# Kernel tuning notes

Measured on AMD Instinct MI355X. Metric: run time of the kernel, lower is better.

Reference implementation:

```python
import jax, jax.numpy as jnp
import numpy as np

B, C, H, W = 4, 512, 56, 56
G, K = 16, 3
P = K * K
GC = C // G
DWK = 3
PAD = 1
OFFSET_SCALE = 1.0


def setup_inputs():
    key = jax.random.key(0)
    ks = jax.random.split(key, 10)

    def w(i, shape, sc=0.02):
        return jax.random.normal(ks[i], shape, jnp.float32) * sc

    return {
        "x": jax.random.normal(ks[0], (B, C, H, W), jnp.float32),
        "w_in": w(1, (C, C)), "b_in": jnp.zeros((C,), jnp.float32),
        "w_dw": w(2, (DWK, DWK, 1, C)), "b_dw": jnp.zeros((C,), jnp.float32),
        "ln_g": jnp.ones((C,), jnp.float32), "ln_b": jnp.zeros((C,), jnp.float32),
        "w_off": w(3, (C, G * P * 2)), "b_off": jnp.zeros((G * P * 2,), jnp.float32),
        "w_mask": w(4, (C, G * P)), "b_mask": jnp.zeros((G * P,), jnp.float32),
        "w_out": w(5, (C, C)), "b_out": jnp.zeros((C,), jnp.float32),
        "bn_g": jnp.ones((C,), jnp.float32), "bn_b": jnp.zeros((C,), jnp.float32),
        "bn_m": w(6, (C,), 0.1), "bn_v": jnp.abs(w(7, (C,), 0.1)) + 1.0,
    }


def _dcnv3_core(xp, offset, mask):
    """xp: [B,H,W,C]; offset: [B,H,W,G*P*2]; mask (softmaxed over P): [B,H,W,G,P]."""
    xpad = jnp.pad(xp, ((0, 0), (PAD, PAD), (PAD, PAD), (0, 0)))
    Hin, Win = H + 2 * PAD, W + 2 * PAD
    # normalized reference points (output-location centers in padded input coords)
    ref_x = (jnp.arange(W, dtype=jnp.float32) + 0.5 + (K - 1) // 2) / Win
    ref_y = (jnp.arange(H, dtype=jnp.float32) + 0.5 + (K - 1) // 2) / Hin
    # dilation grid, kx-major / ky-minor flattening (matches InternImage core)
    k = jnp.arange(K, dtype=jnp.float32) - (K - 1) // 2
    gx = jnp.repeat(k, K) / Win  # [P]
    gy = jnp.tile(k, K) / Hin    # [P]
    off = offset.reshape(B, H, W, G, P, 2)
    lx = ref_x[None, None, :, None, None] + gx * OFFSET_SCALE + off[..., 0] * OFFSET_SCALE / Win
    ly = ref_y[None, :, None, None, None] + gy * OFFSET_SCALE + off[..., 1] * OFFSET_SCALE / Hin
    # grid_sample semantics, align_corners=False, zero padding
    px = lx * Win - 0.5
    py = ly * Hin - 0.5
    x0f = jnp.floor(px)
    y0f = jnp.floor(py)
    tx = px - x0f
    ty = py - y0f
    x0 = x0f.astype(jnp.int32)
    y0 = y0f.astype(jnp.int32)
    flat = xpad.reshape(B, Hin * Win * G, GC)
    gidx = jnp.arange(G)[None, None, :, None]

    def corner(fb, yi, xi):
        valid = (yi >= 0) & (yi < Hin) & (xi >= 0) & (xi < Win)
        idx = (jnp.clip(yi, 0, Hin - 1) * Win + jnp.clip(xi, 0, Win - 1)) * G + gidx
        return jnp.take(fb, idx, axis=0) * valid[..., None]  # [H,W,G,P,GC]

    def sample_one(fb, y0b, x0b, tyb, txb):
        w00 = ((1 - tyb) * (1 - txb))[..., None]
        w01 = ((1 - tyb) * txb)[..., None]
        w10 = (tyb * (1 - txb))[..., None]
        w11 = (tyb * txb)[..., None]
        return (corner(fb, y0b, x0b) * w00 + corner(fb, y0b, x0b + 1) * w01
                + corner(fb, y0b + 1, x0b) * w10 + corner(fb, y0b + 1, x0b + 1) * w11)

    samp = jax.vmap(sample_one)(flat, y0, x0, ty, tx)  # [B,H,W,G,P,GC]
    return jnp.einsum('bhwgpc,bhwgp->bhwgc', samp, mask).reshape(B, H, W, C)


def reference(x, w_in, b_in, w_dw, b_dw, ln_g, ln_b, w_off, b_off, w_mask, b_mask, w_out, b_out, bn_g, bn_b, bn_m, bn_v):
    xh = jnp.transpose(x, (0, 2, 3, 1))  # NCHW -> NHWC
    xp = xh @ w_in + b_in                # input_proj
    # offset/mask branch: depthwise conv + LayerNorm(channels) + GELU
    x1 = jax.lax.conv_general_dilated(xh, w_dw, (1, 1), 'SAME', feature_group_count=C,
                                      dimension_numbers=('NHWC', 'HWIO', 'NHWC')) + b_dw
    mu = x1.mean(-1, keepdims=True)
    var = x1.var(-1, keepdims=True)
    x1 = (x1 - mu) / jnp.sqrt(var + 1e-6) * ln_g + ln_b
    x1 = jax.nn.gelu(x1, approximate=False)
    offset = x1 @ w_off + b_off
    mask = jax.nn.softmax((x1 @ w_mask + b_mask).reshape(B, H, W, G, P), axis=-1)
    y = _dcnv3_core(xp, offset, mask)
    y = y @ w_out + b_out                # output_proj
    y = jnp.transpose(y, (0, 3, 1, 2))   # NHWC -> NCHW
    # BatchNorm2d (inference: running stats) + SiLU
    y = (y - bn_m[:, None, None]) / jnp.sqrt(bn_v[:, None, None] + 1e-5) * bn_g[:, None, None] + bn_b[:, None, None]
    return jax.nn.silu(y)
```

## Files before the change

kernel.cpp:

```cpp
#include <hip/hip_runtime.h>
#include <cmath>

constexpr int B_ = 4, C_ = 512, H_ = 56, W_ = 56;
constexpr int HW_ = H_ * W_;
constexpr int NPIX = B_ * HW_;
constexpr int G_ = 16, P_ = 9;
constexpr int NMSK = G_ * P_;

typedef __attribute__((ext_vector_type(8))) short short8;
typedef __attribute__((ext_vector_type(4))) float f32x4;

__device__ __forceinline__ float b2f(ushort u) {
    union { unsigned int i; float f; } v; v.i = (unsigned int)u << 16; return v.f;
}
__device__ __forceinline__ ushort f2b(float f) {
    unsigned int x = __float_as_uint(f);
    unsigned int r = (x + 0x7fffu + ((x >> 16) & 1u)) >> 16;
    return (ushort)r;
}
__device__ __forceinline__ void gload16(const ushort* g, ushort* l) {
    __builtin_amdgcn_global_load_lds(
        (const __attribute__((address_space(1))) unsigned int*)g,
        (__attribute__((address_space(3))) unsigned int*)l, 16, 0, 0);
}

__global__ __launch_bounds__(256) void prep_weights_kernel(
    const float* __restrict__ w_in, const float* __restrict__ w_off,
    const float* __restrict__ w_mask, const float* __restrict__ w_out,
    const float* __restrict__ b_off, const float* __restrict__ b_mask,
    ushort* __restrict__ wtA, ushort* __restrict__ wtOM, ushort* __restrict__ wtO,
    float* __restrict__ bOM)
{
    __shared__ float tile[32][33];
    int z = blockIdx.z;
    int k0 = blockIdx.x * 32;
    int n0 = blockIdx.y * 32;
    int tx = threadIdx.x, ty = threadIdx.y;
    for (int i = ty; i < 32; i += 8) {
        int k = k0 + i, n = n0 + tx;
        float v;
        if (z == 0) v = w_in[k * 512 + n];
        else if (z == 1) v = w_out[k * 512 + n];
        else v = (n < 288) ? w_off[k * 288 + n]
                           : (n < 432 ? w_mask[k * 144 + (n - 288)] : 0.f);
        tile[i][tx] = v;
    }
    __syncthreads();
    ushort* dst = (z == 0) ? wtA : (z == 1 ? wtO : wtOM);
    for (int i = ty; i < 32; i += 8)
        dst[(size_t)(n0 + i) * 512 + k0 + tx] = f2b(tile[tx][i]);
    if (z == 2 && blockIdx.x == 0 && blockIdx.y == 0) {
        int t = ty * 32 + tx;
        for (int tt = t; tt < 512; tt += 256)
            bOM[tt] = (tt < 288) ? b_off[tt] : (tt < 432 ? b_mask[tt - 288] : 0.f);
    }
}

__global__ __launch_bounds__(256) void transpose_in_kernel(
    const float* __restrict__ in, ushort* __restrict__ out)
{
    __shared__ float tile[32][33];
    int b = blockIdx.z;
    int hw0 = blockIdx.x * 32;
    int c0 = blockIdx.y * 32;
    int tx = threadIdx.x, ty = threadIdx.y;
    const float* ib = in + (size_t)b * C_ * HW_;
    #pragma unroll
    for (int i = ty; i < 32; i += 8)
        tile[i][tx] = ib[(size_t)(c0 + i) * HW_ + hw0 + tx];
    __syncthreads();
    ushort* ob = out + (size_t)b * HW_ * C_;
    #pragma unroll
    for (int i = ty; i < 32; i += 8)
        ob[(size_t)(hw0 + i) * C_ + c0 + tx] = f2b(tile[tx][i]);
}

template <int MODE>
__global__ __launch_bounds__(256) void mfma_gemm_kernel(
    const ushort* __restrict__ A, const ushort* __restrict__ Bt,
    const float* __restrict__ bias, void* __restrict__ Cout,
    const float* __restrict__ bng, const float* __restrict__ bnb,
    const float* __restrict__ bnm, const float* __restrict__ bnv)
{
    __shared__ ushort As[128 * 64];
    __shared__ ushort Bs[128 * 64];
    int tid = threadIdx.x;
    int lane = tid & 63, wid = tid >> 6;
    int bid = blockIdx.x;
    int wgid = (bid & 7) * 49 + (bid >> 3);
    int row0 = (wgid >> 2) * 128, col0 = (wgid & 3) * 128;
    int wm = wid >> 1, wn = wid & 1;

    f32x4 acc[4][4] = {};

    int lr = lane >> 3;
    int sc = (lane & 7) ^ lr;

    for (int k0 = 0; k0 < 512; k0 += 64) {
        if (k0) __syncthreads();
        #pragma unroll
        for (int i = 0; i < 4; i++) {
            int rb = (wid * 4 + i) * 8;
            gload16(A + (size_t)(row0 + rb + lr) * 512 + k0 + sc * 8, &As[rb * 64]);
            gload16(Bt + (size_t)(col0 + rb + lr) * 512 + k0 + sc * 8, &Bs[rb * 64]);
        }
        __syncthreads();
        #pragma unroll
        for (int ks = 0; ks < 2; ks++) {
            short8 af[4], bf[4];
            #pragma unroll
            for (int mi = 0; mi < 4; mi++) {
                int r = wm * 64 + mi * 16 + (lane & 15);
                int c = ((lane >> 4) + ks * 4) ^ (r & 7);
                af[mi] = *(const short8*)((const char*)As + r * 128 + c * 16);
            }
            #pragma unroll
            for (int ni = 0; ni < 4; ni++) {
                int r = wn * 64 + ni * 16 + (lane & 15);
                int c = ((lane >> 4) + ks * 4) ^ (r & 7);
                bf[ni] = *(const short8*)((const char*)Bs + r * 128 + c * 16);
            }
            #pragma unroll
            for (int mi = 0; mi < 4; mi++)
                #pragma unroll
                for (int ni = 0; ni < 4; ni++)
                    acc[mi][ni] = __builtin_amdgcn_mfma_f32_16x16x32_bf16(
                        af[mi], bf[ni], acc[mi][ni], 0, 0, 0);
        }
    }

    if constexpr (MODE == 2) {
        __shared__ float ebuf[4][32][67];
        int n_lane = row0 + wm * 64 + lane;
        int bb = n_lane / HW_;
        int hww = n_lane - bb * HW_;
        size_t obase = (size_t)bb * C_ * HW_ + hww;
        #pragma unroll
        for (int half = 0; half < 2; half++) {
            #pragma unroll
            for (int ni2 = 0; ni2 < 2; ni2++) {
                int ni = half * 2 + ni2;
                int col = col0 + wn * 64 + ni * 16 + (lane & 15);
                float bv = bias[col];
                float inv = rsqrtf(bnv[col] + 1e-5f);
                float bsc = bng[col] * inv;
                float bsh = bnb[col] - bnm[col] * bsc;
                int cl = ni2 * 16 + (lane & 15);
                int rl = (lane >> 4) * 4;
                #pragma unroll
                for (int mi = 0; mi < 4; mi++)
                    #pragma unroll
                    for (int r = 0; r < 4; r++) {
                        float val = acc[mi][ni][r] + bv;
                        float t2 = val * bsc + bsh;
                        float s = t2 / (1.f + expf(-t2));
                        ebuf[wid][cl][mi * 16 + rl + r] = s;
                    }
            }
            __syncthreads();
            #pragma unroll
            for (int c = 0; c < 32; c++) {
                int chan = col0 + wn * 64 + half * 32 + c;
                ((float*)Cout)[obase + (size_t)chan * HW_] = ebuf[wid][c][lane];
            }
            __syncthreads();
        }
    } else {
        #pragma unroll
        for (int ni = 0; ni < 4; ni++) {
            int col = col0 + wn * 64 + ni * 16 + (lane & 15);
            float bv = bias[col];
            #pragma unroll
            for (int mi = 0; mi < 4; mi++) {
                int rowb = row0 + wm * 64 + mi * 16 + (lane >> 4) * 4;
                #pragma unroll
                for (int r = 0; r < 4; r++) {
                    float val = acc[mi][ni][r] + bv;
                    if constexpr (MODE == 0)
                        ((float*)Cout)[(size_t)(rowb + r) * 512 + col] = val;
                    else
                        ((ushort*)Cout)[(size_t)(rowb + r) * 512 + col] = f2b(val);
                }
            }
        }
    }
}

__global__ __launch_bounds__(256) void dwln_kernel(
    const ushort* __restrict__ xh, const float* __restrict__ wdw,
    const float* __restrict__ bdw, const float* __restrict__ lng,
    const float* __restrict__ lnb, ushort* __restrict__ x1)
{
    int tid = threadIdx.x;
    int wid = tid >> 6, lane = tid & 63;
    int bid = blockIdx.x;
    int j = (bid & 7) * (NPIX / 32) + (bid >> 3);
    int n = j * 4 + wid;
    int b = n / HW_, hw = n % HW_;
    int h = hw / W_, w = hw % W_;
    int c0 = lane * 8;
    const ushort* base = xh + (size_t)b * HW_ * C_ + c0;

    uint4 nb[9];
    #pragma unroll
    for (int ky = 0; ky < 3; ky++)
        #pragma unroll
        for (int kx = 0; kx < 3; kx++) {
            int hh = h + ky - 1, ww = w + kx - 1;
            bool ok = (hh >= 0) & (hh < H_) & (ww >= 0) & (ww < W_);
            nb[ky * 3 + kx] = ok ? *(const uint4*)(base + ((size_t)hh * W_ + ww) * C_)
                                 : make_uint4(0u, 0u, 0u, 0u);
        }

    float acc[8];
    {
        float4 b0 = *(const float4*)&bdw[c0];
        float4 b1 = *(const float4*)&bdw[c0 + 4];
        acc[0] = b0.x; acc[1] = b0.y; acc[2] = b0.z; acc[3] = b0.w;
        acc[4] = b1.x; acc[5] = b1.y; acc[6] = b1.z; acc[7] = b1.w;
    }
    #pragma unroll
    for (int p = 0; p < 9; p++) {
        float4 w0 = *(const float4*)&wdw[p * C_ + c0];
        float4 w1 = *(const float4*)&wdw[p * C_ + c0 + 4];
        float wv[8] = {w0.x, w0.y, w0.z, w0.w, w1.x, w1.y, w1.z, w1.w};
        unsigned int u[4] = {nb[p].x, nb[p].y, nb[p].z, nb[p].w};
        #pragma unroll
        for (int q = 0; q < 4; q++) {
            float lo = __uint_as_float(u[q] << 16);
            float hi = __uint_as_float(u[q] & 0xffff0000u);
            acc[2 * q]     += wv[2 * q]     * lo;
            acc[2 * q + 1] += wv[2 * q + 1] * hi;
        }
    }

    float s1 = 0.f, s2 = 0.f;
    #pragma unroll
    for (int q = 0; q < 8; q++) { s1 += acc[q]; s2 += acc[q] * acc[q]; }
    #pragma unroll
    for (int o = 32; o > 0; o >>= 1) {
        s1 += __shfl_xor(s1, o);
        s2 += __shfl_xor(s2, o);
    }
    float mean = s1 * (1.f / 512.f);
    float var = s2 * (1.f / 512.f) - mean * mean;
    float inv = rsqrtf(var + 1e-6f);

    float4 g0 = *(const float4*)&lng[c0];
    float4 g1 = *(const float4*)&lng[c0 + 4];
    float4 e0 = *(const float4*)&lnb[c0];
    float4 e1 = *(const float4*)&lnb[c0 + 4];
    float gv[8] = {g0.x, g0.y, g0.z, g0.w, g1.x, g1.y, g1.z, g1.w};
    float ev[8] = {e0.x, e0.y, e0.z, e0.w, e1.x, e1.y, e1.z, e1.w};
    unsigned int outw[4];
    #pragma unroll
    for (int q = 0; q < 4; q++) {
        float t0 = (acc[2 * q]     - mean) * inv * gv[2 * q]     + ev[2 * q];
        float t1 = (acc[2 * q + 1] - mean) * inv * gv[2 * q + 1] + ev[2 * q + 1];
        float ge0 = 0.5f * t0 * (1.f + erff(t0 * 0.70710678118654752f));
        float ge1 = 0.5f * t1 * (1.f + erff(t1 * 0.70710678118654752f));
        outw[q] = (unsigned int)f2b(ge0) | ((unsigned int)f2b(ge1) << 16);
    }
    *(uint4*)&x1[(size_t)n * C_ + c0] = make_uint4(outw[0], outw[1], outw[2], outw[3]);
}

__global__ __launch_bounds__(256) void dcn_sample_kernel(
    const ushort* __restrict__ xp, const ushort* __restrict__ om,
    ushort* __restrict__ y1)
{
    __shared__ float slog[NMSK];
    __shared__ float sw4[NMSK][4];
    __shared__ int   sa4[NMSK][4];
    int bid = blockIdx.x;
    int n = (bid & 7) * (NPIX / 8) + (bid >> 3);
    int b = n / HW_, hw = n % HW_;
    int h = hw / W_, w = hw % W_;
    int tid = threadIdx.x;
    const ushort* omp = om + (size_t)n * 512;

    if (tid < NMSK) slog[tid] = b2f(omp[288 + tid]);
    __syncthreads();
    if (tid < G_) {
        float mx = -1e30f;
        #pragma unroll
        for (int p = 0; p < P_; p++) mx = fmaxf(mx, slog[tid * P_ + p]);
        float e[P_], s = 0.f;
        #pragma unroll
        for (int p = 0; p < P_; p++) { e[p] = expf(slog[tid * P_ + p] - mx); s += e[p]; }
        float invs = 1.f / s;
        #pragma unroll
        for (int p = 0; p < P_; p++) slog[tid * P_ + p] = e[p] * invs;
    }
    __syncthreads();
    if (tid < NMSK) {
        int g = tid / 9, p = tid - g * 9;
        float ox = b2f(omp[g * 18 + p * 2 + 0]);
        float oy = b2f(omp[g * 18 + p * 2 + 1]);
        float px = (float)(w + (p / 3)) + ox;
        float py = (float)(h + (p % 3)) + oy;
        float x0f = floorf(px), y0f = floorf(py);
        float tx = px - x0f, ty = py - y0f;
        int x0 = (int)x0f, y0 = (int)y0f;
        float m = slog[tid];
        float ww[4] = { (1.f - ty) * (1.f - tx) * m, (1.f - ty) * tx * m,
                        ty * (1.f - tx) * m,         ty * tx * m };
        #pragma unroll
        for (int i = 0; i < 4; i++) {
            int yy = y0 + (i >> 1), xx = x0 + (i & 1);
            bool valid = (yy >= 1 && yy <= H_ && xx >= 1 && xx <= W_);
            sa4[tid][i] = valid ? ((yy - 1) * W_ + (xx - 1)) * C_ : 0;
            sw4[tid][i] = valid ? ww[i] : 0.f;
        }
    }
    __syncthreads();

    const ushort* xpb = xp + (size_t)b * HW_ * C_;
    int c0 = tid * 2;
    int g = tid >> 4;

    int addr[P_][4];
    #pragma unroll
    for (int p = 0; p < P_; p++)
        #pragma unroll
        for (int i = 0; i < 4; i++)
            addr[p][i] = sa4[g * 9 + p][i] + c0;

    unsigned int v[P_][4];
    #pragma unroll
    for (int p = 0; p < P_; p++)
        #pragma unroll
        for (int i = 0; i < 4; i++)
            v[p][i] = *(const unsigned int*)(xpb + addr[p][i]);

    float ax = 0.f, ay = 0.f;
    #pragma unroll
    for (int p = 0; p < P_; p++)
        #pragma unroll
        for (int i = 0; i < 4; i++) {
            float wgt = sw4[g * 9 + p][i];
            float lo = __uint_as_float(v[p][i] << 16);
            float hi = __uint_as_float(v[p][i] & 0xffff0000u);
            ax += wgt * lo;
            ay += wgt * hi;
        }

    ushort2 o; o.x = f2b(ax); o.y = f2b(ay);
    *(ushort2*)&y1[(size_t)n * 512 + c0] = o;
}

extern "C" void kernel_launch(void* const* d_in, const int* in_sizes, int n_in,
                              void* d_out, int out_size, void* d_ws, size_t ws_size,
                              hipStream_t stream)
{
    const float* x      = (const float*)d_in[0];
    const float* w_in   = (const float*)d_in[1];
    const float* b_in   = (const float*)d_in[2];
    const float* w_dw   = (const float*)d_in[3];
    const float* b_dw   = (const float*)d_in[4];
    const float* ln_g   = (const float*)d_in[5];
    const float* ln_b   = (const float*)d_in[6];
    const float* w_off  = (const float*)d_in[7];
    const float* b_off  = (const float*)d_in[8];
    const float* w_mask = (const float*)d_in[9];
    const float* b_mask = (const float*)d_in[10];
    const float* w_out  = (const float*)d_in[11];
    const float* b_out  = (const float*)d_in[12];
    const float* bn_g   = (const float*)d_in[13];
    const float* bn_b   = (const float*)d_in[14];
    const float* bn_m   = (const float*)d_in[15];
    const float* bn_v   = (const float*)d_in[16];
    float* out = (float*)d_out;

    const size_t NC = (size_t)NPIX * C_;
    char* wsp = (char*)d_ws;
    ushort* xh  = (ushort*)wsp;  wsp += NC * 2;
    ushort* x1  = (ushort*)wsp;  wsp += NC * 2;
    ushort* xpb = (ushort*)wsp;  wsp += NC * 2;
    ushort* om  = (ushort*)wsp;  wsp += NC * 2;
    ushort* wtA = (ushort*)wsp;  wsp += 512 * 512 * 2;
    ushort* wtOM= (ushort*)wsp;  wsp += 512 * 512 * 2;
    ushort* wtO = (ushort*)wsp;  wsp += 512 * 512 * 2;
    float*  bOM = (float*)wsp;   wsp += 512 * 4;

    dim3 tb(32, 8);
    prep_weights_kernel<<<dim3(16, 16, 3), tb, 0, stream>>>(
        w_in, w_off, w_mask, w_out, b_off, b_mask, wtA, wtOM, wtO, bOM);

    transpose_in_kernel<<<dim3(HW_ / 32, C_ / 32, B_), tb, 0, stream>>>(x, xh);

    mfma_gemm_kernel<1><<<392, 256, 0, stream>>>(
        xh, wtA, b_in, xpb, nullptr, nullptr, nullptr, nullptr);

    dwln_kernel<<<NPIX / 4, 256, 0, stream>>>(xh, w_dw, b_dw, ln_g, ln_b, x1);

    mfma_gemm_kernel<1><<<392, 256, 0, stream>>>(
        x1, wtOM, bOM, om, nullptr, nullptr, nullptr, nullptr);

    dcn_sample_kernel<<<NPIX, 256, 0, stream>>>(xpb, om, x1 );

    mfma_gemm_kernel<2><<<392, 256, 0, stream>>>(
        x1, wtO, b_out, out, bn_g, bn_b, bn_m, bn_v);
}
```

Before: 114.2 us.

## Co-launch input projection GEMM and depthwise-LN in one grid

Merges the input-projection GEMM and the depthwise conv + LayerNorm + GELU kernel into a single launch, with block ID deciding which body a block runs. Both read only xh, so they can overlap on the GPU and one launch plus its tail is saved. GEMM shared memory is now a union of the tile buffers and the epilogue buffer, and an extra barrier is added before reuse. The side effect is that dwln blocks now reserve the larger GEMM LDS allocation, which may reduce their occupancy.

```diff
diff --git a/kernel.cpp b/kernel.cpp
--- a/kernel.cpp
+++ b/kernel.cpp
@@ -6,6 +6,7 @@
 constexpr int NPIX = B_ * HW_;
 constexpr int G_ = 16, P_ = 9;
 constexpr int NMSK = G_ * P_;
+constexpr int GEMM_BLOCKS = 392;
 
 typedef __attribute__((ext_vector_type(8))) short short8;
 typedef __attribute__((ext_vector_type(4))) float f32x4;
@@ -23,6 +24,11 @@
         (const __attribute__((address_space(1))) unsigned int*)g,
         (__attribute__((address_space(3))) unsigned int*)l, 16, 0, 0);
 }
+
+union GemmSMem {
+    struct { ushort As[128 * 64]; ushort Bs[128 * 64]; } s;
+    float eb[4][32][67];
+};
 
 __global__ __launch_bounds__(256) void prep_weights_kernel(
     const float* __restrict__ w_in, const float* __restrict__ w_off,
@@ -76,18 +82,15 @@
 }
 
 template <int MODE>
-__global__ __launch_bounds__(256) void mfma_gemm_kernel(
-    const ushort* __restrict__ A, const ushort* __restrict__ Bt,
+__device__ __forceinline__ void gemm_body(
+    ushort* __restrict__ As, ushort* __restrict__ Bs, float* __restrict__ ebf,
+    int wgid, const ushort* __restrict__ A, const ushort* __restrict__ Bt,
     const float* __restrict__ bias, void* __restrict__ Cout,
     const float* __restrict__ bng, const float* __restrict__ bnb,
     const float* __restrict__ bnm, const float* __restrict__ bnv)
 {
-    __shared__ ushort As[128 * 64];
-    __shared__ ushort Bs[128 * 64];
     int tid = threadIdx.x;
     int lane = tid & 63, wid = tid >> 6;
-    int bid = blockIdx.x;
-    int wgid = (bid & 7) * 49 + (bid >> 3);
     int row0 = (wgid >> 2) * 128, col0 = (wgid & 3) * 128;
     int wm = wid >> 1, wn = wid & 1;
 
@@ -130,7 +133,7 @@
     }
 
     if constexpr (MODE == 2) {
-        __shared__ float ebuf[4][32][67];
+        __syncthreads();
         int n_lane = row0 + wm * 64 + lane;
         int bb = n_lane / HW_;
         int hww = n_lane - bb * HW_;
@@ -154,14 +157,15 @@
                         float val = acc[mi][ni][r] + bv;
                         float t2 = val * bsc + bsh;
                         float s = t2 / (1.f + expf(-t2));
-                        ebuf[wid][cl][mi * 16 + rl + r] = s;
+                        ebf[((wid * 32) + cl) * 67 + mi * 16 + rl + r] = s;
                     }
             }
             __syncthreads();
             #pragma unroll
             for (int c = 0; c < 32; c++) {
                 int chan = col0 + wn * 64 + half * 32 + c;
-                ((float*)Cout)[obase + (size_t)chan * HW_] = ebuf[wid][c][lane];
+                ((float*)Cout)[obase + (size_t)chan * HW_] =
+                    ebf[((wid * 32) + c) * 67 + lane];
             }
             __syncthreads();
         }
@@ -186,14 +190,27 @@
     }
 }
 
-__global__ __launch_bounds__(256) void dwln_kernel(
-    const ushort* __restrict__ xh, const float* __restrict__ wdw,
+template <int MODE>
+__global__ __launch_bounds__(256) void mfma_gemm_kernel(
+    const ushort* __restrict__ A, const ushort* __restrict__ Bt,
+    const float* __restrict__ bias, void* __restrict__ Cout,
+    const float* __restrict__ bng, const float* __restrict__ bnb,
+    const float* __restrict__ bnm, const float* __restrict__ bnv)
+{
+    __shared__ GemmSMem sm;
+    int bid = blockIdx.x;
+    int wgid = (bid & 7) * 49 + (bid >> 3);
+    gemm_body<MODE>(sm.s.As, sm.s.Bs, &sm.eb[0][0][0], wgid,
+                    A, Bt, bias, Cout, bng, bnb, bnm, bnv);
+}
+
+__device__ __forceinline__ void dwln_body(
+    int bid, const ushort* __restrict__ xh, const float* __restrict__ wdw,
     const float* __restrict__ bdw, const float* __restrict__ lng,
     const float* __restrict__ lnb, ushort* __restrict__ x1)
 {
     int tid = threadIdx.x;
     int wid = tid >> 6, lane = tid & 63;
-    int bid = blockIdx.x;
     int j = (bid & 7) * (NPIX / 32) + (bid >> 3);
     int n = j * 4 + wid;
     int b = n / HW_, hw = n % HW_;
@@ -262,6 +279,24 @@
         outw[q] = (unsigned int)f2b(ge0) | ((unsigned int)f2b(ge1) << 16);
     }
     *(uint4*)&x1[(size_t)n * C_ + c0] = make_uint4(outw[0], outw[1], outw[2], outw[3]);
+}
+
+__global__ __launch_bounds__(256) void g1_dwln_kernel(
+    const ushort* __restrict__ xh, const ushort* __restrict__ wtA,
+    const float* __restrict__ b_in, ushort* __restrict__ xpb,
+    const float* __restrict__ wdw, const float* __restrict__ bdw,
+    const float* __restrict__ lng, const float* __restrict__ lnb,
+    ushort* __restrict__ x1)
+{
+    __shared__ GemmSMem sm;
+    int bid = blockIdx.x;
+    if (bid < GEMM_BLOCKS) {
+        int wgid = (bid & 7) * 49 + (bid >> 3);
+        gemm_body<1>(sm.s.As, sm.s.Bs, &sm.eb[0][0][0], wgid,
+                     xh, wtA, b_in, xpb, nullptr, nullptr, nullptr, nullptr);
+    } else {
+        dwln_body(bid - GEMM_BLOCKS, xh, wdw, bdw, lng, lnb, x1);
+    }
 }
 
 __global__ __launch_bounds__(256) void dcn_sample_kernel(
@@ -388,16 +423,14 @@
 
     transpose_in_kernel<<<dim3(HW_ / 32, C_ / 32, B_), tb, 0, stream>>>(x, xh);
 
-    mfma_gemm_kernel<1><<<392, 256, 0, stream>>>(
-        xh, wtA, b_in, xpb, nullptr, nullptr, nullptr, nullptr);
-
-    dwln_kernel<<<NPIX / 4, 256, 0, stream>>>(xh, w_dw, b_dw, ln_g, ln_b, x1);
-
-    mfma_gemm_kernel<1><<<392, 256, 0, stream>>>(
+    g1_dwln_kernel<<<GEMM_BLOCKS + NPIX / 4, 256, 0, stream>>>(
+        xh, wtA, b_in, xpb, w_dw, b_dw, ln_g, ln_b, x1);
+
+    mfma_gemm_kernel<1><<<GEMM_BLOCKS, 256, 0, stream>>>(
         x1, wtOM, bOM, om, nullptr, nullptr, nullptr, nullptr);
 
     dcn_sample_kernel<<<NPIX, 256, 0, stream>>>(xpb, om, x1 );
 
-    mfma_gemm_kernel<2><<<392, 256, 0, stream>>>(
+    mfma_gemm_kernel<2><<<GEMM_BLOCKS, 256, 0, stream>>>(
         x1, wtO, b_out, out, bn_g, bn_b, bn_m, bn_v);
 }
```

After: 112.0 us. No clear change (-1.9%).
